# Kernel optimization log

Hardware: AMD Instinct MI355X
Metric: run time of the kernel (lower is better)

Reference implementation:

```python
import jax, jax.numpy as jnp
import numpy as np

ALPHA = 0.25
GAMMA = 2.0
W_CLASS = 2.0
W_BBOX = 5.0
W_GIOU = 2.0
EPS_LOG = 1e-8
EPS_DIV = 1e-6


def box_cxcywh_to_xyxy(b):
    cx, cy, w, h = b[..., 0], b[..., 1], b[..., 2], b[..., 3]
    return jnp.stack([cx - 0.5 * w, cy - 0.5 * h, cx + 0.5 * w, cy + 0.5 * h], axis=-1)


def generalized_box_iou(b1, b2):
    # b1: [N,4], b2: [M,4], xyxy -> giou [N,M]
    area1 = (b1[:, 2] - b1[:, 0]) * (b1[:, 3] - b1[:, 1])
    area2 = (b2[:, 2] - b2[:, 0]) * (b2[:, 3] - b2[:, 1])
    lt = jnp.maximum(b1[:, None, :2], b2[None, :, :2])
    rb = jnp.minimum(b1[:, None, 2:], b2[None, :, 2:])
    wh = jnp.maximum(rb - lt, 0.0)
    inter = wh[..., 0] * wh[..., 1]
    union = area1[:, None] + area2[None, :] - inter
    iou = inter / jnp.maximum(union, EPS_DIV)
    lt_e = jnp.minimum(b1[:, None, :2], b2[None, :, :2])
    rb_e = jnp.maximum(b1[:, None, 2:], b2[None, :, 2:])
    wh_e = jnp.maximum(rb_e - lt_e, 0.0)
    enclosing = wh_e[..., 0] * wh_e[..., 1]
    return iou - (enclosing - union) / jnp.maximum(enclosing, EPS_DIV)


def setup_inputs() -> dict:
    key = jax.random.key(0)
    k1, k2, k3, k4 = jax.random.split(key, 4)
    B, Q, C, T = 16, 900, 91, 4800  # T = 16 images * 300 targets
    pred_logits = jax.random.normal(k1, (B, Q, C), dtype=jnp.float32)
    pred_boxes = jax.random.uniform(k2, (B, Q, 4), dtype=jnp.float32)  # cxcywh in [0,1]
    tgt_ids = jax.random.randint(k3, (T,), 1, C + 1)  # 1-based labels (code uses tgt_ids - 1)
    tgt_boxes = jax.random.uniform(k4, (T, 4), dtype=jnp.float32)
    return {"pred_logits": pred_logits, "pred_boxes": pred_boxes,
            "tgt_ids": tgt_ids, "tgt_boxes": tgt_boxes}


def reference(pred_logits, pred_boxes, tgt_ids, tgt_boxes):
    B, Q, C = pred_logits.shape
    pl = jax.nn.sigmoid(pred_logits.reshape(B * Q, C))   # [BQ, C]
    pb = pred_boxes.reshape(B * Q, 4)                    # [BQ, 4]

    # focal-style class cost
    neg_cost = (1.0 - ALPHA) * pl ** GAMMA * (-jnp.log(1.0 - pl + EPS_LOG))
    pos_cost = ALPHA * (1.0 - pl) ** GAMMA * (-jnp.log(pl + EPS_LOG))
    cost_class = (pos_cost - neg_cost)[:, tgt_ids - 1]   # [BQ, T]

    # L1 box cost (cdist, p=1)
    cost_bbox = jnp.sum(jnp.abs(pb[:, None, :] - tgt_boxes[None, :, :]), axis=-1)  # [BQ, T]

    # negative generalized IoU cost
    cost_giou = -generalized_box_iou(box_cxcywh_to_xyxy(pb), box_cxcywh_to_xyxy(tgt_boxes))

    Cmat = W_CLASS * cost_class + W_BBOX * cost_bbox + W_GIOU * cost_giou
    return Cmat.reshape(B, Q, -1)  # [B, Q, T]
```

## Files before the change

### kernel.cpp

```cpp
#include <hip/hip_runtime.h>

constexpr int kB = 16, kQ = 900, kC = 91, kT = 4800;
constexpr int kBQ = kB * kQ;
constexpr int kTI = 16;
constexpr int kJT = 4;
constexpr int kBT = 256;
constexpr int kJB = kBT * kJT;

__global__ __launch_bounds__(256)
void class_cost_kernel(const float* __restrict__ logits,
                       float* __restrict__ cd, int n) {
    int idx = blockIdx.x * 256 + threadIdx.x;
    if (idx >= n) return;
    float x = logits[idx];
    float p = 1.0f / (1.0f + expf(-x));
    float omp = 1.0f - p;
    float pos = 0.25f * omp * omp * (-logf(p + 1e-8f));
    float neg = 0.75f * p * p * (-logf(omp + 1e-8f));
    cd[idx] = 2.0f * (pos - neg);
}

__global__ __launch_bounds__(256)
void cost_kernel(const float* __restrict__ pred_boxes,
                 const int*   __restrict__ tgt_ids,
                 const float* __restrict__ tgt_boxes,
                 const float* __restrict__ cd,
                 float*       __restrict__ out) {
    __shared__ float  lds_cd[kTI * kC];
    __shared__ float4 lds_pb[kTI];

    const int tid = threadIdx.x;
    const int i0  = blockIdx.y * kTI;
    const int j0  = blockIdx.x * kJB + tid * kJT;
    const bool valid = (j0 + kJT <= kT);

    for (int k = tid; k < kTI * kC; k += kBT)
        lds_cd[k] = cd[i0 * kC + k];
    if (tid < kTI)
        lds_pb[tid] = reinterpret_cast<const float4*>(pred_boxes)[i0 + tid];
    __syncthreads();

    float tcx[kJT], tcy[kJT], tw[kJT], th[kJT];
    float tx0[kJT], ty0[kJT], tx1[kJT], ty1[kJT], ta[kJT];
    int   tco[kJT];
    if (valid) {
        int4 ids = *reinterpret_cast<const int4*>(&tgt_ids[j0]);
        tco[0] = ids.x - 1; tco[1] = ids.y - 1; tco[2] = ids.z - 1; tco[3] = ids.w - 1;
        #pragma unroll
        for (int q = 0; q < kJT; ++q) {
            float4 tb = reinterpret_cast<const float4*>(tgt_boxes)[j0 + q];
            tcx[q] = tb.x; tcy[q] = tb.y; tw[q] = tb.z; th[q] = tb.w;
            tx0[q] = tb.x - 0.5f * tb.z;  ty0[q] = tb.y - 0.5f * tb.w;
            tx1[q] = tb.x + 0.5f * tb.z;  ty1[q] = tb.y + 0.5f * tb.w;
            ta[q]  = tb.z * tb.w;
        }
    } else {
        #pragma unroll
        for (int q = 0; q < kJT; ++q) {
            tcx[q] = tcy[q] = tw[q] = th[q] = 0.f;
            tx0[q] = ty0[q] = tx1[q] = ty1[q] = ta[q] = 0.f;
            tco[q] = 0;
        }
    }

    for (int ii = 0; ii < kTI; ++ii) {
        const float4 pb = lds_pb[ii];
        const float pcx = pb.x, pcy = pb.y, pw = pb.z, ph = pb.w;
        const float px0 = pcx - 0.5f * pw, py0 = pcy - 0.5f * ph;
        const float px1 = pcx + 0.5f * pw, py1 = pcy + 0.5f * ph;
        const float pa  = pw * ph;

        float4 res;
        #pragma unroll
        for (int q = 0; q < kJT; ++q) {
            float cdv = lds_cd[ii * kC + tco[q]];

            float l1 = fabsf(pcx - tcx[q]) + fabsf(pcy - tcy[q])
                     + fabsf(pw  - tw[q] ) + fabsf(ph  - th[q] );

            float lx = fmaxf(px0, tx0[q]), ly = fmaxf(py0, ty0[q]);
            float rx = fminf(px1, tx1[q]), ry = fminf(py1, ty1[q]);
            float iw = fmaxf(rx - lx, 0.f), ih = fmaxf(ry - ly, 0.f);
            float inter = iw * ih;
            float uni   = pa + ta[q] - inter;
            float iou   = inter * __builtin_amdgcn_rcpf(fmaxf(uni, 1e-6f));

            float ex0 = fminf(px0, tx0[q]), ey0 = fminf(py0, ty0[q]);
            float ex1 = fmaxf(px1, tx1[q]), ey1 = fmaxf(py1, ty1[q]);
            float ew  = fmaxf(ex1 - ex0, 0.f), eh = fmaxf(ey1 - ey0, 0.f);
            float enc = ew * eh;
            float giou = iou - (enc - uni) * __builtin_amdgcn_rcpf(fmaxf(enc, 1e-6f));

            float c = cdv + 5.0f * l1 - 2.0f * giou;
            (&res.x)[q] = c;
        }

        if (valid) {
            size_t off = (size_t)(i0 + ii) * kT + j0;
            *reinterpret_cast<float4*>(&out[off]) = res;
        }
    }
}

extern "C" void kernel_launch(void* const* d_in, const int* in_sizes, int n_in,
                              void* d_out, int out_size, void* d_ws, size_t ws_size,
                              hipStream_t stream) {
    const float* logits  = (const float*)d_in[0];
    const float* pboxes  = (const float*)d_in[1];
    const int*   tids    = (const int*)d_in[2];
    const float* tboxes  = (const float*)d_in[3];
    float* out = (float*)d_out;
    float* cd  = (float*)d_ws;

    const int n_cd = kBQ * kC;
    class_cost_kernel<<<(n_cd + 255) / 256, 256, 0, stream>>>(logits, cd, n_cd);

    dim3 grid((kT + kJB - 1) / kJB, kBQ / kTI);
    cost_kernel<<<grid, 256, 0, stream>>>(pboxes, tids, tboxes, cd, out);
}
```

Before: 314.7 us.

## Transpose class-cost LDS tile, vectorize gathers, simplify GIoU, use nontemporal stores

Stores the per-block class-cost tile in LDS transposed (class-major, padded stride 20). Each thread can then fetch four query rows for a target class with a single 16-byte LDS read instead of one scalar gather per query. The GIoU enclosing box is derived algebraically from the intersection extents, which drops the min/max ops, and the output is written with nontemporal vector stores. The early return for out-of-range threads is placed after the barrier, so it is safe. The kernel is likely bound by output writes, so the gains from the ALU and LDS changes may be limited. The algebraic enclosing box also skips the clamp to zero, which changes results slightly for degenerate boxes.

```diff
diff --git a/kernel.cpp b/kernel.cpp
--- a/kernel.cpp
+++ b/kernel.cpp
@@ -1,4 +1,6 @@
 #include <hip/hip_runtime.h>
+
+typedef float f32x4 __attribute__((ext_vector_type(4)));
 
 constexpr int kB = 16, kQ = 900, kC = 91, kT = 4800;
 constexpr int kBQ = kB * kQ;
@@ -6,6 +8,7 @@
 constexpr int kJT = 4;
 constexpr int kBT = 256;
 constexpr int kJB = kBT * kJT;
+constexpr int kCDS = 20;
 
 __global__ __launch_bounds__(256)
 void class_cost_kernel(const float* __restrict__ logits,
@@ -26,78 +29,85 @@
                  const float* __restrict__ tgt_boxes,
                  const float* __restrict__ cd,
                  float*       __restrict__ out) {
-    __shared__ float  lds_cd[kTI * kC];
+    __shared__ float  lds_cdT[kC * kCDS];
     __shared__ float4 lds_pb[kTI];
 
     const int tid = threadIdx.x;
     const int i0  = blockIdx.y * kTI;
     const int j0  = blockIdx.x * kJB + tid * kJT;
-    const bool valid = (j0 + kJT <= kT);
 
-    for (int k = tid; k < kTI * kC; k += kBT)
-        lds_cd[k] = cd[i0 * kC + k];
+    for (int k = tid; k < kTI * kC; k += kBT) {
+        int i = k / kC, c = k - i * kC;
+        lds_cdT[c * kCDS + i] = cd[(i0 + i) * kC + c];
+    }
     if (tid < kTI)
         lds_pb[tid] = reinterpret_cast<const float4*>(pred_boxes)[i0 + tid];
     __syncthreads();
 
+    if (j0 + kJT > kT) return;
+
+    int4 ids = *reinterpret_cast<const int4*>(&tgt_ids[j0]);
+    int tco[kJT] = {ids.x - 1, ids.y - 1, ids.z - 1, ids.w - 1};
     float tcx[kJT], tcy[kJT], tw[kJT], th[kJT];
     float tx0[kJT], ty0[kJT], tx1[kJT], ty1[kJT], ta[kJT];
-    int   tco[kJT];
-    if (valid) {
-        int4 ids = *reinterpret_cast<const int4*>(&tgt_ids[j0]);
-        tco[0] = ids.x - 1; tco[1] = ids.y - 1; tco[2] = ids.z - 1; tco[3] = ids.w - 1;
-        #pragma unroll
-        for (int q = 0; q < kJT; ++q) {
-            float4 tb = reinterpret_cast<const float4*>(tgt_boxes)[j0 + q];
-            tcx[q] = tb.x; tcy[q] = tb.y; tw[q] = tb.z; th[q] = tb.w;
-            tx0[q] = tb.x - 0.5f * tb.z;  ty0[q] = tb.y - 0.5f * tb.w;
-            tx1[q] = tb.x + 0.5f * tb.z;  ty1[q] = tb.y + 0.5f * tb.w;
-            ta[q]  = tb.z * tb.w;
-        }
-    } else {
-        #pragma unroll
-        for (int q = 0; q < kJT; ++q) {
-            tcx[q] = tcy[q] = tw[q] = th[q] = 0.f;
-            tx0[q] = ty0[q] = tx1[q] = ty1[q] = ta[q] = 0.f;
-            tco[q] = 0;
-        }
+    #pragma unroll
+    for (int q = 0; q < kJT; ++q) {
+        float4 tb = reinterpret_cast<const float4*>(tgt_boxes)[j0 + q];
+        tcx[q] = tb.x; tcy[q] = tb.y; tw[q] = tb.z; th[q] = tb.w;
+        tx0[q] = tb.x - 0.5f * tb.z;  ty0[q] = tb.y - 0.5f * tb.w;
+        tx1[q] = tb.x + 0.5f * tb.z;  ty1[q] = tb.y + 0.5f * tb.w;
+        ta[q]  = tb.z * tb.w;
     }
 
-    for (int ii = 0; ii < kTI; ++ii) {
-        const float4 pb = lds_pb[ii];
-        const float pcx = pb.x, pcy = pb.y, pw = pb.z, ph = pb.w;
-        const float px0 = pcx - 0.5f * pw, py0 = pcy - 0.5f * ph;
-        const float px1 = pcx + 0.5f * pw, py1 = pcy + 0.5f * ph;
-        const float pa  = pw * ph;
+    const size_t row0 = (size_t)i0 * kT + j0;
 
-        float4 res;
+    #pragma unroll 1
+    for (int ig = 0; ig < kTI / 4; ++ig) {
+        f32x4 cdv[kJT];
         #pragma unroll
-        for (int q = 0; q < kJT; ++q) {
-            float cdv = lds_cd[ii * kC + tco[q]];
+        for (int q = 0; q < kJT; ++q)
+            cdv[q] = *reinterpret_cast<const f32x4*>(
+                         &lds_cdT[tco[q] * kCDS + ig * 4]);
 
-            float l1 = fabsf(pcx - tcx[q]) + fabsf(pcy - tcy[q])
-                     + fabsf(pw  - tw[q] ) + fabsf(ph  - th[q] );
+        #pragma unroll
+        for (int i2 = 0; i2 < 4; ++i2) {
+            const int ii = ig * 4 + i2;
+            const float4 pb = lds_pb[ii];
+            const float pcx = pb.x, pcy = pb.y, pw = pb.z, ph = pb.w;
+            const float px0 = pcx - 0.5f * pw, py0 = pcy - 0.5f * ph;
+            const float px1 = pcx + 0.5f * pw, py1 = pcy + 0.5f * ph;
+            const float pa  = pw * ph;
 
-            float lx = fmaxf(px0, tx0[q]), ly = fmaxf(py0, ty0[q]);
-            float rx = fminf(px1, tx1[q]), ry = fminf(py1, ty1[q]);
-            float iw = fmaxf(rx - lx, 0.f), ih = fmaxf(ry - ly, 0.f);
-            float inter = iw * ih;
-            float uni   = pa + ta[q] - inter;
-            float iou   = inter * __builtin_amdgcn_rcpf(fmaxf(uni, 1e-6f));
+            f32x4 res;
+            #pragma unroll
+            for (int q = 0; q < kJT; ++q) {
+                const float cdvq = cdv[q][i2];
 
-            float ex0 = fminf(px0, tx0[q]), ey0 = fminf(py0, ty0[q]);
-            float ex1 = fmaxf(px1, tx1[q]), ey1 = fmaxf(py1, ty1[q]);
-            float ew  = fmaxf(ex1 - ex0, 0.f), eh = fmaxf(ey1 - ey0, 0.f);
-            float enc = ew * eh;
-            float giou = iou - (enc - uni) * __builtin_amdgcn_rcpf(fmaxf(enc, 1e-6f));
+                float dx = pcx - tcx[q], dy = pcy - tcy[q];
+                float dw = pw  - tw[q],  dh = ph  - th[q];
+                float l1 = (fabsf(dx) + fabsf(dy)) + (fabsf(dw) + fabsf(dh));
 
-            float c = cdv + 5.0f * l1 - 2.0f * giou;
-            (&res.x)[q] = c;
-        }
+                float lx = fmaxf(px0, tx0[q]), ly = fmaxf(py0, ty0[q]);
+                float rx = fminf(px1, tx1[q]), ry = fminf(py1, ty1[q]);
+                float iwr = rx - lx, ihr = ry - ly;
+                float inter = fmaxf(iwr, 0.f) * fmaxf(ihr, 0.f);
 
-        if (valid) {
-            size_t off = (size_t)(i0 + ii) * kT + j0;
-            *reinterpret_cast<float4*>(&out[off]) = res;
+                float ew  = (pw + tw[q]) - iwr;
+                float eh  = (ph + th[q]) - ihr;
+                float enc = ew * eh;
+                float uni = (pa + ta[q]) - inter;
+
+                float rcpu = __builtin_amdgcn_rcpf(fmaxf(uni, 1e-6f));
+                float rcpe = __builtin_amdgcn_rcpf(fmaxf(enc, 1e-6f));
+
+                float c = fmaf(5.0f, l1, cdvq);
+                c = fmaf(-2.0f, inter * rcpu, c);
+                c = fmaf( 2.0f, (enc - uni) * rcpe, c);
+                res[q] = c;
+            }
+
+            __builtin_nontemporal_store(res,
+                reinterpret_cast<f32x4*>(&out[row0 + (size_t)ii * kT]));
         }
     }
 }
```

Measured after the change: 308.0 us. -2.1%, faster.
